# Kernel tuning notes

Measured on AMD Instinct MI355X. Metric: run time of the kernel, lower is better.

## Reference

```python
import jax, jax.numpy as jnp
import numpy as np

HIGH_THRESHOLD = 0.1
EPS = 1e-6


def _gaussian_kernel_2d(ksize=5, sigma=1.0):
    x = np.arange(ksize, dtype=np.float32) - ksize // 2
    g = np.exp(-(x * x) / (2.0 * sigma * sigma))
    g = g / g.sum()
    return (g[:, None] * g[None, :]).astype(np.float32)  # (5,5)


def _sobel_kernels():
    gx = np.array([[-1.0, 0.0, 1.0], [-2.0, 0.0, 2.0], [-1.0, 0.0, 1.0]], np.float32)
    gy = gx.T.copy()
    return np.stack([gx, gy])[:, None]  # (2,1,3,3)


def _nms_kernels():
    # kornia get_canny_nms_kernel: 8 direction kernels, center 1, -1 at neighbor
    k = np.zeros((8, 1, 3, 3), np.float32)
    k[:, 0, 1, 1] = 1.0
    offs = [(1, 2), (0, 2), (0, 1), (0, 0), (1, 0), (2, 0), (2, 1), (2, 2)]
    for i, (r, c) in enumerate(offs):
        k[i, 0, r, c] = -1.0
    return k


def _conv(x, w, pad, mode=None):
    # x: (B,Cin,H,W), w: (Cout,Cin,kh,kw)
    if mode is not None:
        x = jnp.pad(x, ((0, 0), (0, 0), (pad, pad), (pad, pad)), mode=mode)
        padding = 'VALID'
    else:
        padding = [(pad, pad), (pad, pad)]
    return jax.lax.conv_general_dilated(
        x, w, (1, 1), padding, dimension_numbers=('NCHW', 'OIHW', 'NCHW'))


def cal_edge(x):
    dt = x.dtype
    if x.shape[1] == 3:  # rgb_to_grayscale
        w = jnp.array([0.299, 0.587, 0.114], dt).reshape(1, 3, 1, 1)
        x = jnp.sum(x * w, axis=1, keepdims=True)
    # gaussian_blur2d, reflect border (kornia default)
    blurred = _conv(x, jnp.asarray(_gaussian_kernel_2d())[None, None], 2, mode='reflect')
    # spatial_gradient (sobel, replicate border)
    grads = _conv(blurred, jnp.asarray(_sobel_kernels()), 1, mode='edge')  # (B,2,H,W)
    gx, gy = grads[:, 0:1], grads[:, 1:2]
    magnitude = jnp.sqrt(gx * gx + gy * gy + EPS)  # (B,1,H,W)
    angle = jnp.arctan2(gy, gx) * (180.0 / np.pi)
    angle = jnp.round(angle / 45.0) * 45.0
    nms_mag = _conv(magnitude, jnp.asarray(_nms_kernels()), 1)  # (B,8,H,W), zero pad
    pos_idx = jnp.mod(angle / 45.0, 8.0).astype(jnp.int32)        # (B,1,H,W)
    neg_idx = jnp.mod(angle / 45.0 + 4.0, 8.0).astype(jnp.int32)
    cp = jnp.take_along_axis(nms_mag, pos_idx, axis=1)
    cn = jnp.take_along_axis(nms_mag, neg_idx, axis=1)
    is_max = jnp.minimum(cp, cn) > 0.0
    magnitude = magnitude * is_max
    # F.threshold(mag, high, 0); then F.threshold(-e, -high, -1); e = -e
    e1 = jnp.where(magnitude > HIGH_THRESHOLD, magnitude, jnp.zeros((), dt))
    edges = -jnp.where(-e1 > -HIGH_THRESHOLD, -e1, jnp.full((), -1.0, dt))
    return edges


def setup_inputs() -> dict:
    key = jax.random.key(0)
    k1, k2 = jax.random.split(key)
    shape = (8, 3, 1024, 1024)
    op = jax.random.uniform(k1, shape, jnp.float32)
    gt = jax.random.uniform(k2, shape, jnp.float32)
    return {'op': op, 'gt': gt}


def reference(op, gt):
    edge_op = cal_edge(op)
    edge_gt = cal_edge(gt)
    return jnp.mean(jnp.abs(edge_op - edge_gt))
```

## Files before the change

### kernel.cpp

```cpp
#include <hip/hip_runtime.h>

#define N 1024
#define NN (N * N)
#define STRIPS 19
#define SEGS 32
#define SEGROWS 32
#define NWAVES (STRIPS * SEGS * 8)

__device__ __forceinline__ int refl(int i) {
    if (i < 0) return -i;
    if (i >= N) return 2 * N - 2 - i;
    return i;
}

__global__ __launch_bounds__(64)
void edge_diff_kernel(const float* __restrict__ op, const float* __restrict__ gt,
                      unsigned int* __restrict__ partials)
{
    const float w0 = 0.05448868f, w1 = 0.24420134f, w2 = 0.40261996f,
                w3 = 0.24420134f, w4 = 0.05448868f;

    int b = blockIdx.x;
    int img   = b / (STRIPS * SEGS);
    int rem   = b - img * (STRIPS * SEGS);
    int strip = rem / SEGS;
    int seg   = rem - strip * SEGS;
    int lane  = threadIdx.x;

    int cb = strip * 56 - 4;
    int c  = cb + lane;
    int cR = refl(c);

    const float* A = op + (size_t)img * 3 * NN;
    const float* B = gt + (size_t)img * 3 * NN;

    const bool cz0 = (c == 0), czN = (c == N - 1);
    const bool valid = (lane >= 4) && (lane <= 59) && (c >= 0) && (c < N);

    const int iL1 = lane - 1, iL2 = lane - 2, iR1 = lane + 1, iR2 = lane + 2;

    float ha0=0,ha1=0,ha2=0,ha3=0,ha4=0;
    float bla0=0,bla1=0,bla2=0;
    float mga0=0,mga1=0,mga2=0;
    float mgla0=0,mgla1=0,mgla2=0;
    float mgra0=0,mgra1=0,mgra2=0;
    int   axa = 0;
    float hb0=0,hb1=0,hb2=0,hb3=0,hb4=0;
    float blb0=0,blb1=0,blb2=0;
    float mgb0=0,mgb1=0,mgb2=0;
    float mglb0=0,mglb1=0,mglb2=0;
    float mgrb0=0,mgrb1=0,mgrb2=0;
    int   axb = 0;

    int acc = 0;
    const int R0 = seg * SEGROWS;

#pragma unroll 4
    for (int y = R0 - 4; y <= R0 + 35; ++y) {
        int rr = refl(y);
        const float* pa = A + (size_t)rr * N + cR;
        const float* pb = B + (size_t)rr * N + cR;

        float ga = 0.299f * pa[0] + 0.587f * pa[NN] + 0.114f * pa[2 * NN];
        float gb = 0.299f * pb[0] + 0.587f * pb[NN] + 0.114f * pb[2 * NN];

        float gal2 = __shfl(ga, iL2, 64), gal1 = __shfl(ga, iL1, 64);
        float gar1 = __shfl(ga, iR1, 64), gar2 = __shfl(ga, iR2, 64);
        float gbl2 = __shfl(gb, iL2, 64), gbl1 = __shfl(gb, iL1, 64);
        float gbr1 = __shfl(gb, iR1, 64), gbr2 = __shfl(gb, iR2, 64);
        float hna = w0*gal2 + w1*gal1 + w2*ga + w3*gar1 + w4*gar2;
        float hnb = w0*gbl2 + w1*gbl1 + w2*gb + w3*gbr1 + w4*gbr2;
        ha0=ha1; ha1=ha2; ha2=ha3; ha3=ha4; ha4=hna;
        hb0=hb1; hb1=hb2; hb2=hb3; hb3=hb4; hb4=hnb;

        float bna = w0*ha0 + w1*ha1 + w2*ha2 + w3*ha3 + w4*ha4;
        float bnb = w0*hb0 + w1*hb1 + w2*hb2 + w3*hb3 + w4*hb4;
        bla0=bla1; bla1=bla2; bla2=bna;
        blb0=blb1; blb1=blb2; blb2=bnb;

        int z = y - 3;
        float Ara = (z == 0)     ? bla1 : bla0;
        float Cra = (z == N - 1) ? bla1 : bla2;
        float Arb = (z == 0)     ? blb1 : blb0;
        float Crb = (z == N - 1) ? blb1 : blb2;

        float sa = Ara + 2.f*bla1 + Cra;  float da = Cra - Ara;
        float sb = Arb + 2.f*blb1 + Crb;  float db = Crb - Arb;

        float sal = __shfl(sa, iL1, 64), sar = __shfl(sa, iR1, 64);
        float dal = __shfl(da, iL1, 64), dar = __shfl(da, iR1, 64);
        float sbl = __shfl(sb, iL1, 64), sbr = __shfl(sb, iR1, 64);
        float dbl = __shfl(db, iL1, 64), dbr = __shfl(db, iR1, 64);
        sal = cz0 ? sa : sal;  dal = cz0 ? da : dal;
        sar = czN ? sa : sar;  dar = czN ? da : dar;
        sbl = cz0 ? sb : sbl;  dbl = cz0 ? db : dbl;
        sbr = czN ? sb : sbr;  dbr = czN ? db : dbr;

        float gxa = sar - sal;            float gya = dal + 2.f*da + dar;
        float gxb = sbr - sbl;            float gyb = dbl + 2.f*db + dbr;
        float maga = sqrtf(gxa*gxa + gya*gya + 1e-6f);
        float magb = sqrtf(gxb*gxb + gyb*gyb + 1e-6f);

        float axx = fabsf(gxa), ayy = fabsf(gya);
        int cda = (ayy <= 0.41421356f * axx) ? 0
                : (ayy >= 2.41421356f * axx) ? 1
                : (((gxa > 0.f) == (gya > 0.f)) ? 2 : 3);
        float bxx = fabsf(gxb), byy = fabsf(gyb);
        int cdb = (byy <= 0.41421356f * bxx) ? 0
                : (byy >= 2.41421356f * bxx) ? 1
                : (((gxb > 0.f) == (gyb > 0.f)) ? 2 : 3);

        float mala = __shfl(maga, iL1, 64); mala = cz0 ? 0.f : mala;
        float mara = __shfl(maga, iR1, 64); mara = czN ? 0.f : mara;
        float malb = __shfl(magb, iL1, 64); malb = cz0 ? 0.f : malb;
        float marb = __shfl(magb, iR1, 64); marb = czN ? 0.f : marb;

        mga0=mga1;   mga1=mga2;   mga2=maga;
        mgla0=mgla1; mgla1=mgla2; mgla2=mala;
        mgra0=mgra1; mgra1=mgra2; mgra2=mara;
        mgb0=mgb1;   mgb1=mgb2;   mgb2=magb;
        mglb0=mglb1; mglb1=mglb2; mglb2=malb;
        mgrb0=mgrb1; mgrb1=mgrb2; mgrb2=marb;

        int axUa = axa; axa = cda;
        int axUb = axb; axb = cdb;

        if (y >= R0 + 4) {
            int w = y - 4;
            float m0a = mga0, l0a = mgla0, r0a = mgra0;
            float m2a = mga2, l2a = mgla2, r2a = mgra2;
            float m0b = mgb0, l0b = mglb0, r0b = mgrb0;
            float m2b = mgb2, l2b = mglb2, r2b = mgrb2;
            if (w == 0)     { m0a=0; l0a=0; r0a=0; m0b=0; l0b=0; r0b=0; }
            if (w == N - 1) { m2a=0; l2a=0; r2a=0; m2b=0; l2b=0; r2b=0; }

            float n1a = (axUa == 0) ? mgra1 : (axUa == 1) ? m0a : (axUa == 2) ? r0a : l0a;
            float n2a = (axUa == 0) ? mgla1 : (axUa == 1) ? m2a : (axUa == 2) ? l2a : r2a;
            float n1b = (axUb == 0) ? mgrb1 : (axUb == 1) ? m0b : (axUb == 2) ? r0b : l0b;
            float n2b = (axUb == 0) ? mglb1 : (axUb == 1) ? m2b : (axUb == 2) ? l2b : r2b;

            bool ea = (mga1 > n1a) && (mga1 > n2a) && (mga1 > 0.1f);
            bool eb = (mgb1 > n1b) && (mgb1 > n2b) && (mgb1 > 0.1f);
            acc += (int)(valid && (ea != eb));
        }
    }

    for (int off = 32; off > 0; off >>= 1)
        acc += __shfl_down(acc, off, 64);
    if (lane == 0)
        partials[b] = (unsigned int)acc;
}

__global__ __launch_bounds__(256)
void finalize_kernel(const unsigned int* __restrict__ partials, float* __restrict__ out)
{
    __shared__ unsigned int ws[4];
    int tid = threadIdx.x;
    unsigned int sum = 0;
    for (int i = tid; i < NWAVES; i += 256)
        sum += partials[i];
    int d = (int)sum;
    for (int off = 32; off > 0; off >>= 1)
        d += __shfl_down(d, off, 64);
    if ((tid & 63) == 0) ws[tid >> 6] = (unsigned int)d;
    __syncthreads();
    if (tid == 0)
        out[0] = (float)(ws[0] + ws[1] + ws[2] + ws[3]) / 8388608.0f;
}

extern "C" void kernel_launch(void* const* d_in, const int* in_sizes, int n_in,
                              void* d_out, int out_size, void* d_ws, size_t ws_size,
                              hipStream_t stream)
{
    const float* op = (const float*)d_in[0];
    const float* gt = (const float*)d_in[1];
    unsigned int* partials = (unsigned int*)d_ws;

    edge_diff_kernel<<<dim3(NWAVES), dim3(64), 0, stream>>>(op, gt, partials);
    finalize_kernel<<<1, dim3(256), 0, stream>>>(partials, (float*)d_out);
}
```

Baseline: 232.9 us.

## Specialize edge kernel for interior and border tiles, peel warmup rows

Uses templates to split the work units into interior, column-border, row-border and corner classes, so interior tiles skip the reflect and replicate boundary selects. The warmup rows that only prime the sliding window are peeled into their own loop without the NMS branch. Four wavefronts are now packed per 256-thread block instead of one per block. This cuts per-row ALU and branch overhead, at the cost of more code size and a remapping of units to tiles that must still cover every tile exactly once.

```diff
diff --git a/kernel.cpp b/kernel.cpp
--- a/kernel.cpp
+++ b/kernel.cpp
@@ -5,7 +5,12 @@
 #define STRIPS 19
 #define SEGS 32
 #define SEGROWS 32
-#define NWAVES (STRIPS * SEGS * 8)
+#define NUNITS (STRIPS * SEGS * 8)
+
+#define U_INT 4080
+#define U_COL 480
+#define U_ROW 272
+#define U_COR 32
 
 __device__ __forceinline__ int refl(int i) {
     if (i < 0) return -i;
@@ -13,29 +18,109 @@
     return i;
 }
 
-__global__ __launch_bounds__(64)
-void edge_diff_kernel(const float* __restrict__ op, const float* __restrict__ gt,
-                      unsigned int* __restrict__ partials)
+#define ROW_BODY(yv, DO_NMS)                                                      \
+  {                                                                               \
+    int rr = ROWE ? refl(yv) : (yv);                                              \
+    const float* ra = A + (size_t)rr * N;      \
+    const float* rb = B + (size_t)rr * N;                                         \
+    float ga = 0.299f * ra[cR] + 0.587f * ra[cR + NN] + 0.114f * ra[cR + 2 * NN]; \
+    float gb = 0.299f * rb[cR] + 0.587f * rb[cR + NN] + 0.114f * rb[cR + 2 * NN]; \
+    float gal2 = __shfl(ga, iL2, 64), gal1 = __shfl(ga, iL1, 64);                 \
+    float gar1 = __shfl(ga, iR1, 64), gar2 = __shfl(ga, iR2, 64);                 \
+    float gbl2 = __shfl(gb, iL2, 64), gbl1 = __shfl(gb, iL1, 64);                 \
+    float gbr1 = __shfl(gb, iR1, 64), gbr2 = __shfl(gb, iR2, 64);                 \
+    float hna = w0*gal2 + w1*gal1 + w2*ga + w3*gar1 + w4*gar2;                    \
+    float hnb = w0*gbl2 + w1*gbl1 + w2*gb + w3*gbr1 + w4*gbr2;                    \
+    ha0=ha1; ha1=ha2; ha2=ha3; ha3=ha4; ha4=hna;                                  \
+    hb0=hb1; hb1=hb2; hb2=hb3; hb3=hb4; hb4=hnb;                                  \
+    float bna = w0*ha0 + w1*ha1 + w2*ha2 + w3*ha3 + w4*ha4;                       \
+    float bnb = w0*hb0 + w1*hb1 + w2*hb2 + w3*hb3 + w4*hb4;                       \
+    bla0=bla1; bla1=bla2; bla2=bna;                                               \
+    blb0=blb1; blb1=blb2; blb2=bnb;                                               \
+    float Ara, Cra, Arb, Crb;                                                     \
+    if (ROWE) {                                                                   \
+      int z = (yv) - 3;                                                           \
+      Ara = (z == 0)     ? bla1 : bla0;                                           \
+      Cra = (z == N - 1) ? bla1 : bla2;                                           \
+      Arb = (z == 0)     ? blb1 : blb0;                                           \
+      Crb = (z == N - 1) ? blb1 : blb2;                                           \
+    } else { Ara = bla0; Cra = bla2; Arb = blb0; Crb = blb2; }                    \
+    float sa = Ara + 2.f*bla1 + Cra;  float da = Cra - Ara;                       \
+    float sb = Arb + 2.f*blb1 + Crb;  float db = Crb - Arb;                       \
+    float sal = __shfl(sa, iL1, 64), sar = __shfl(sa, iR1, 64);                   \
+    float dal = __shfl(da, iL1, 64), dar = __shfl(da, iR1, 64);                   \
+    float sbl = __shfl(sb, iL1, 64), sbr = __shfl(sb, iR1, 64);                   \
+    float dbl = __shfl(db, iL1, 64), dbr = __shfl(db, iR1, 64);                   \
+    if (COLE) {                                                                   \
+      sal = cz0 ? sa : sal;  dal = cz0 ? da : dal;                                \
+      sar = czN ? sa : sar;  dar = czN ? da : dar;                                \
+      sbl = cz0 ? sb : sbl;  dbl = cz0 ? db : dbl;                                \
+      sbr = czN ? sb : sbr;  dbr = czN ? db : dbr;                                \
+    }                                                                             \
+    float gxa = sar - sal;            float gya = dal + 2.f*da + dar;             \
+    float gxb = sbr - sbl;            float gyb = dbl + 2.f*db + dbr;             \
+    float maga = sqrtf(gxa*gxa + gya*gya + 1e-6f);                                \
+    float magb = sqrtf(gxb*gxb + gyb*gyb + 1e-6f);                                \
+    float axx = fabsf(gxa), ayy = fabsf(gya);                                     \
+    int cda = (ayy <= 0.41421356f * axx) ? 0                                      \
+            : (ayy >= 2.41421356f * axx) ? 1                                      \
+            : (((gxa > 0.f) == (gya > 0.f)) ? 2 : 3);                             \
+    float bxx = fabsf(gxb), byy = fabsf(gyb);                                     \
+    int cdb = (byy <= 0.41421356f * bxx) ? 0                                      \
+            : (byy >= 2.41421356f * bxx) ? 1                                      \
+            : (((gxb > 0.f) == (gyb > 0.f)) ? 2 : 3);                             \
+    float mala = __shfl(maga, iL1, 64); if (COLE) mala = cz0 ? 0.f : mala;        \
+    float mara = __shfl(maga, iR1, 64); if (COLE) mara = czN ? 0.f : mara;        \
+    float malb = __shfl(magb, iL1, 64); if (COLE) malb = cz0 ? 0.f : malb;        \
+    float marb = __shfl(magb, iR1, 64); if (COLE) marb = czN ? 0.f : marb;        \
+    mga0=mga1;   mga1=mga2;   mga2=maga;                                          \
+    mgla0=mgla1; mgla1=mgla2; mgla2=mala;                                         \
+    mgra0=mgra1; mgra1=mgra2; mgra2=mara;                                         \
+    mgb0=mgb1;   mgb1=mgb2;   mgb2=magb;                                          \
+    mglb0=mglb1; mglb1=mglb2; mglb2=malb;                                         \
+    mgrb0=mgrb1; mgrb1=mgrb2; mgrb2=marb;                                         \
+    int axUa = axa; axa = cda;                                                    \
+    int axUb = axb; axb = cdb;                                                    \
+    if (DO_NMS) {                                                                 \
+      float m0a = mga0, l0a = mgla0, r0a = mgra0;                                 \
+      float m2a = mga2, l2a = mgla2, r2a = mgra2;                                 \
+      float m0b = mgb0, l0b = mglb0, r0b = mgrb0;                                 \
+      float m2b = mgb2, l2b = mglb2, r2b = mgrb2;                                 \
+      if (ROWE) {                                                                 \
+        int w = (yv) - 4;                                                         \
+        if (w == 0)     { m0a=0; l0a=0; r0a=0; m0b=0; l0b=0; r0b=0; }             \
+        if (w == N - 1) { m2a=0; l2a=0; r2a=0; m2b=0; l2b=0; r2b=0; }             \
+      }                                                                           \
+      float n1a = (axUa == 0) ? mgra1 : (axUa == 1) ? m0a : (axUa == 2) ? r0a : l0a; \
+      float n2a = (axUa == 0) ? mgla1 : (axUa == 1) ? m2a : (axUa == 2) ? l2a : r2a; \
+      float n1b = (axUb == 0) ? mgrb1 : (axUb == 1) ? m0b : (axUb == 2) ? r0b : l0b; \
+      float n2b = (axUb == 0) ? mglb1 : (axUb == 1) ? m2b : (axUb == 2) ? l2b : r2b; \
+      bool ea = (mga1 > n1a) && (mga1 > n2a) && (mga1 > 0.1f);                    \
+      bool eb = (mgb1 > n1b) && (mgb1 > n2b) && (mgb1 > 0.1f);                    \
+      acc += (int)(valid && (ea != eb));                                          \
+    }                                                                             \
+  }
+
+template<bool COLE, bool ROWE>
+__device__ __forceinline__ void edge_unit(
+    const float* __restrict__ op, const float* __restrict__ gt,
+    unsigned int* __restrict__ partials,
+    int unit, int img, int strip, int seg, int lane)
 {
     const float w0 = 0.05448868f, w1 = 0.24420134f, w2 = 0.40261996f,
                 w3 = 0.24420134f, w4 = 0.05448868f;
 
-    int b = blockIdx.x;
-    int img   = b / (STRIPS * SEGS);
-    int rem   = b - img * (STRIPS * SEGS);
-    int strip = rem / SEGS;
-    int seg   = rem - strip * SEGS;
-    int lane  = threadIdx.x;
-
     int cb = strip * 56 - 4;
     int c  = cb + lane;
-    int cR = refl(c);
+    int cR = COLE ? refl(c) : c;
 
     const float* A = op + (size_t)img * 3 * NN;
     const float* B = gt + (size_t)img * 3 * NN;
 
-    const bool cz0 = (c == 0), czN = (c == N - 1);
-    const bool valid = (lane >= 4) && (lane <= 59) && (c >= 0) && (c < N);
+    const bool cz0 = COLE && (c == 0);
+    const bool czN = COLE && (c == N - 1);
+    const bool valid = (lane >= 4) && (lane <= 59) &&
+                       (!COLE || ((c >= 0) && (c < N)));
 
     const int iL1 = lane - 1, iL2 = lane - 2, iR1 = lane + 1, iR2 = lane + 2;
 
@@ -56,99 +141,48 @@
     const int R0 = seg * SEGROWS;
 
 #pragma unroll 4
-    for (int y = R0 - 4; y <= R0 + 35; ++y) {
-        int rr = refl(y);
-        const float* pa = A + (size_t)rr * N + cR;
-        const float* pb = B + (size_t)rr * N + cR;
-
-        float ga = 0.299f * pa[0] + 0.587f * pa[NN] + 0.114f * pa[2 * NN];
-        float gb = 0.299f * pb[0] + 0.587f * pb[NN] + 0.114f * pb[2 * NN];
-
-        float gal2 = __shfl(ga, iL2, 64), gal1 = __shfl(ga, iL1, 64);
-        float gar1 = __shfl(ga, iR1, 64), gar2 = __shfl(ga, iR2, 64);
-        float gbl2 = __shfl(gb, iL2, 64), gbl1 = __shfl(gb, iL1, 64);
-        float gbr1 = __shfl(gb, iR1, 64), gbr2 = __shfl(gb, iR2, 64);
-        float hna = w0*gal2 + w1*gal1 + w2*ga + w3*gar1 + w4*gar2;
-        float hnb = w0*gbl2 + w1*gbl1 + w2*gb + w3*gbr1 + w4*gbr2;
-        ha0=ha1; ha1=ha2; ha2=ha3; ha3=ha4; ha4=hna;
-        hb0=hb1; hb1=hb2; hb2=hb3; hb3=hb4; hb4=hnb;
-
-        float bna = w0*ha0 + w1*ha1 + w2*ha2 + w3*ha3 + w4*ha4;
-        float bnb = w0*hb0 + w1*hb1 + w2*hb2 + w3*hb3 + w4*hb4;
-        bla0=bla1; bla1=bla2; bla2=bna;
-        blb0=blb1; blb1=blb2; blb2=bnb;
-
-        int z = y - 3;
-        float Ara = (z == 0)     ? bla1 : bla0;
-        float Cra = (z == N - 1) ? bla1 : bla2;
-        float Arb = (z == 0)     ? blb1 : blb0;
-        float Crb = (z == N - 1) ? blb1 : blb2;
-
-        float sa = Ara + 2.f*bla1 + Cra;  float da = Cra - Ara;
-        float sb = Arb + 2.f*blb1 + Crb;  float db = Crb - Arb;
-
-        float sal = __shfl(sa, iL1, 64), sar = __shfl(sa, iR1, 64);
-        float dal = __shfl(da, iL1, 64), dar = __shfl(da, iR1, 64);
-        float sbl = __shfl(sb, iL1, 64), sbr = __shfl(sb, iR1, 64);
-        float dbl = __shfl(db, iL1, 64), dbr = __shfl(db, iR1, 64);
-        sal = cz0 ? sa : sal;  dal = cz0 ? da : dal;
-        sar = czN ? sa : sar;  dar = czN ? da : dar;
-        sbl = cz0 ? sb : sbl;  dbl = cz0 ? db : dbl;
-        sbr = czN ? sb : sbr;  dbr = czN ? db : dbr;
-
-        float gxa = sar - sal;            float gya = dal + 2.f*da + dar;
-        float gxb = sbr - sbl;            float gyb = dbl + 2.f*db + dbr;
-        float maga = sqrtf(gxa*gxa + gya*gya + 1e-6f);
-        float magb = sqrtf(gxb*gxb + gyb*gyb + 1e-6f);
-
-        float axx = fabsf(gxa), ayy = fabsf(gya);
-        int cda = (ayy <= 0.41421356f * axx) ? 0
-                : (ayy >= 2.41421356f * axx) ? 1
-                : (((gxa > 0.f) == (gya > 0.f)) ? 2 : 3);
-        float bxx = fabsf(gxb), byy = fabsf(gyb);
-        int cdb = (byy <= 0.41421356f * bxx) ? 0
-                : (byy >= 2.41421356f * bxx) ? 1
-                : (((gxb > 0.f) == (gyb > 0.f)) ? 2 : 3);
-
-        float mala = __shfl(maga, iL1, 64); mala = cz0 ? 0.f : mala;
-        float mara = __shfl(maga, iR1, 64); mara = czN ? 0.f : mara;
-        float malb = __shfl(magb, iL1, 64); malb = cz0 ? 0.f : malb;
-        float marb = __shfl(magb, iR1, 64); marb = czN ? 0.f : marb;
-
-        mga0=mga1;   mga1=mga2;   mga2=maga;
-        mgla0=mgla1; mgla1=mgla2; mgla2=mala;
-        mgra0=mgra1; mgra1=mgra2; mgra2=mara;
-        mgb0=mgb1;   mgb1=mgb2;   mgb2=magb;
-        mglb0=mglb1; mglb1=mglb2; mglb2=malb;
-        mgrb0=mgrb1; mgrb1=mgrb2; mgrb2=marb;
-
-        int axUa = axa; axa = cda;
-        int axUb = axb; axb = cdb;
-
-        if (y >= R0 + 4) {
-            int w = y - 4;
-            float m0a = mga0, l0a = mgla0, r0a = mgra0;
-            float m2a = mga2, l2a = mgla2, r2a = mgra2;
-            float m0b = mgb0, l0b = mglb0, r0b = mgrb0;
-            float m2b = mgb2, l2b = mglb2, r2b = mgrb2;
-            if (w == 0)     { m0a=0; l0a=0; r0a=0; m0b=0; l0b=0; r0b=0; }
-            if (w == N - 1) { m2a=0; l2a=0; r2a=0; m2b=0; l2b=0; r2b=0; }
-
-            float n1a = (axUa == 0) ? mgra1 : (axUa == 1) ? m0a : (axUa == 2) ? r0a : l0a;
-            float n2a = (axUa == 0) ? mgla1 : (axUa == 1) ? m2a : (axUa == 2) ? l2a : r2a;
-            float n1b = (axUb == 0) ? mgrb1 : (axUb == 1) ? m0b : (axUb == 2) ? r0b : l0b;
-            float n2b = (axUb == 0) ? mglb1 : (axUb == 1) ? m2b : (axUb == 2) ? l2b : r2b;
-
-            bool ea = (mga1 > n1a) && (mga1 > n2a) && (mga1 > 0.1f);
-            bool eb = (mgb1 > n1b) && (mgb1 > n2b) && (mgb1 > 0.1f);
-            acc += (int)(valid && (ea != eb));
-        }
-    }
+    for (int y = R0 - 4; y < R0 + 4; ++y) ROW_BODY(y, 0)
+
+#pragma unroll 4
+    for (int y = R0 + 4; y <= R0 + 35; ++y) ROW_BODY(y, 1)
 
     for (int off = 32; off > 0; off >>= 1)
         acc += __shfl_down(acc, off, 64);
     if (lane == 0)
-        partials[b] = (unsigned int)acc;
+        partials[unit] = (unsigned int)acc;
+}
+
+__global__ __launch_bounds__(256)
+void edge_diff_kernel(const float* __restrict__ op, const float* __restrict__ gt,
+                      unsigned int* __restrict__ partials)
+{
+    int lane = threadIdx.x & 63;
+    int unit = blockIdx.x * 4 + (threadIdx.x >> 6);
+
+    if (unit < U_INT) {
+        int u = unit;
+        int img = u / 510; int r = u - img * 510;
+        int strip = 1 + r / 30, seg = 1 + r % 30;
+        edge_unit<false, false>(op, gt, partials, unit, img, strip, seg, lane);
+    } else if (unit < U_INT + U_COL) {
+        int u = unit - U_INT;
+        int img = u / 60; int r = u - img * 60;
+        int strip = (r >= 30) ? 18 : 0;
+        int seg   = 1 + (r >= 30 ? r - 30 : r);
+        edge_unit<true, false>(op, gt, partials, unit, img, strip, seg, lane);
+    } else if (unit < U_INT + U_COL + U_ROW) {
+        int u = unit - (U_INT + U_COL);
+        int img = u / 34; int r = u - img * 34;
+        int strip = 1 + (r >> 1);
+        int seg   = (r & 1) ? 31 : 0;
+        edge_unit<false, true>(op, gt, partials, unit, img, strip, seg, lane);
+    } else {
+        int u = unit - (U_INT + U_COL + U_ROW);
+        int img = u >> 2; int r = u & 3;
+        int strip = (r >> 1) ? 18 : 0;
+        int seg   = (r & 1) ? 31 : 0;
+        edge_unit<true, true>(op, gt, partials, unit, img, strip, seg, lane);
+    }
 }
 
 __global__ __launch_bounds__(256)
@@ -157,7 +191,7 @@
     __shared__ unsigned int ws[4];
     int tid = threadIdx.x;
     unsigned int sum = 0;
-    for (int i = tid; i < NWAVES; i += 256)
+    for (int i = tid; i < NUNITS; i += 256)
         sum += partials[i];
     int d = (int)sum;
     for (int off = 32; off > 0; off >>= 1)
@@ -176,6 +210,6 @@
     const float* gt = (const float*)d_in[1];
     unsigned int* partials = (unsigned int*)d_ws;
 
-    edge_diff_kernel<<<dim3(NWAVES), dim3(64), 0, stream>>>(op, gt, partials);
+    edge_diff_kernel<<<dim3(NUNITS / 4), dim3(256), 0, stream>>>(op, gt, partials);
     finalize_kernel<<<1, dim3(256), 0, stream>>>(partials, (float*)d_out);
 }
```

Result: slower. 240.5 us (+3.2%).
